# Performance work log

Hardware: AMD Instinct MI355X
Metric: run time of the kernel (lower is better)

The kernel has to match this reference:

```python
import jax, jax.numpy as jnp
import numpy as np


def setup_inputs() -> dict:
    key = jax.random.key(0)
    ks = jax.random.split(key, 16)
    s = 0.02
    return {
        "video": jax.random.normal(ks[0], (256, 10, 7, 7, 512), jnp.float32),
        "audio": jax.random.normal(ks[1], (10, 256, 128), jnp.float32),
        "Wv1": jax.random.normal(ks[2], (512, 512), jnp.float32) * s,
        "bv1": jnp.zeros((512,), jnp.float32),
        "Wa1": jax.random.normal(ks[3], (512, 128), jnp.float32) * s,
        "ba1": jnp.zeros((512,), jnp.float32),
        "Wb": jax.random.normal(ks[4], (256, 512), jnp.float32) * s,
        "bb": jnp.zeros((256,), jnp.float32),
        "Wc": jax.random.normal(ks[5], (512, 256), jnp.float32) * s,
        "bc": jnp.zeros((512,), jnp.float32),
        "Wv2": jax.random.normal(ks[6], (256, 512), jnp.float32) * s,
        "bv2": jnp.zeros((256,), jnp.float32),
        "Wa2": jax.random.normal(ks[7], (256, 128), jnp.float32) * s,
        "ba2": jnp.zeros((256,), jnp.float32),
        "Ws": jax.random.normal(ks[8], (1, 256), jnp.float32) * s,
        "bs": jnp.zeros((1,), jnp.float32),
    }


def reference(video, audio, Wv1, bv1, Wa1, ba1, Wb, bb, Wc, bc, Wv2, bv2, Wa2, ba2, Ws, bs):
    # video: [B, T, H, W, 512]; audio: [T, B, 128] (transposed inside, as in torch code)
    relu = jax.nn.relu
    audio = jnp.transpose(audio, (1, 0, 2))                  # [B, T, 128]
    B, T, H, W, Vd = video.shape
    BT, HW = B * T, H * W
    af = audio.reshape(BT, -1)                               # [BT, 128]
    vf = video.reshape(B, T, HW, Vd)                         # raw visual feature

    # channel attention
    aq1 = relu(af @ Wa1.T + ba1)[:, None, :]                 # [BT, 1, 512]
    vq1 = relu(vf @ Wv1.T + bv1).reshape(BT, HW, -1)         # [BT, 49, 512]
    avq = jnp.mean(aq1 * vq1, axis=-2)                       # [BT, 512]
    avq = relu(avq @ Wb.T + bb)                              # [BT, 256]
    c_att_maps = jax.nn.sigmoid(avq @ Wc.T + bc).reshape(B, T, 1, Vd)
    c_att = (vf * (c_att_maps + 1.0)).reshape(BT, HW, Vd)    # [BT, 49, 512]

    # spatial attention
    cq = relu(c_att @ Wv2.T + bv2)                           # [BT, 49, 256]
    aq2 = relu(af @ Wa2.T + ba2)[:, None, :]                 # [BT, 1, 256]
    logits = jnp.tanh((cq * aq2) @ Ws.T + bs)                # [BT, 49, 1]
    s_att = jax.nn.softmax(jnp.transpose(logits, (0, 2, 1)), axis=-1)  # [BT, 1, 49]

    out = jnp.matmul(s_att, c_att)                           # [BT, 1, 512]
    return out.reshape(B, T, Vd)
```

## Files before the change

kernel.cpp:

```cpp
#include <hip/hip_runtime.h>

typedef __bf16 bf16x8 __attribute__((ext_vector_type(8)));
typedef float f32x4 __attribute__((ext_vector_type(4)));

__device__ __forceinline__ unsigned short f2bf(float f) {
    union { float f; unsigned int u; } x; x.f = f;
    unsigned int r = x.u + 0x7FFFu + ((x.u >> 16) & 1u);
    return (unsigned short)(r >> 16);
}
__device__ __forceinline__ float bf2f(unsigned short v) {
    union { unsigned int u; float f; } x; x.u = ((unsigned int)v) << 16; return x.f;
}
__device__ __forceinline__ float bf2f_lo(unsigned int w) {
    union { unsigned int u; float f; } x; x.u = w << 16; return x.f;
}
__device__ __forceinline__ float bf2f_hi(unsigned int w) {
    union { unsigned int u; float f; } x; x.u = w & 0xffff0000u; return x.f;
}
__device__ __forceinline__ unsigned int cvt_pk_bf16(float lo, float hi) {
    unsigned int r;
    asm("v_cvt_pk_bf16_f32 %0, %1, %2" : "=v"(r) : "v"(lo), "v"(hi));
    return r;
}
__device__ __forceinline__ void async16(const void* g, void* l) {
    __builtin_amdgcn_global_load_lds(
        (const __attribute__((address_space(1))) unsigned int*)g,
        (__attribute__((address_space(3))) unsigned int*)l, 16, 0, 0);
}

__global__ __launch_bounds__(256) void k_prep(
    const float* __restrict__ Wv1, const float* __restrict__ Wv2,
    unsigned short* __restrict__ Wv1bf, unsigned short* __restrict__ Wv2bf)
{
    int idx = blockIdx.x * 256 + threadIdx.x;
    if (idx < 262144) {
        Wv1bf[idx] = f2bf(Wv1[idx]);
    } else {
        int j = idx - 262144;
        Wv2bf[j] = f2bf(Wv2[j]);
    }
}

__global__ __launch_bounds__(256) void k_prepv(
    const float* __restrict__ v, unsigned short* __restrict__ vbf)
{
    const size_t stride = (size_t)gridDim.x * 256;
    for (size_t c = (size_t)blockIdx.x * 256 + threadIdx.x; c < 8028160u; c += stride) {
        const float* p = v + c * 8;
        float4 a = *(const float4*)p;
        float4 b = *(const float4*)(p + 4);
        uint4 o;
        o.x = cvt_pk_bf16(a.x, a.y); o.y = cvt_pk_bf16(a.z, a.w);
        o.z = cvt_pk_bf16(b.x, b.y); o.w = cvt_pk_bf16(b.z, b.w);
        *(uint4*)(vbf + c * 8) = o;
    }
}

__global__ __launch_bounds__(256) void k_audio(
    const float* __restrict__ audio,
    const float* __restrict__ Wa1, const float* __restrict__ ba1,
    const float* __restrict__ Wa2, const float* __restrict__ ba2,
    float* __restrict__ aq1, float* __restrict__ aq2)
{
    __shared__ float afs[4][128];
    const int btBase = blockIdx.x * 4;
    const int tid = threadIdx.x;
    for (int i = tid; i < 512; i += 256) {
        int g = i >> 7, k = i & 127;
        int bt = btBase + g;
        int b = bt / 10, t = bt - b * 10;
        afs[g][k] = audio[(t * 256 + b) * 128 + k];
    }
    __syncthreads();
    const int c = tid;
    float a1a[4] = {0.f,0.f,0.f,0.f}, a1b[4] = {0.f,0.f,0.f,0.f}, a2[4] = {0.f,0.f,0.f,0.f};
    const float* w1a = Wa1 + c * 128;
    const float* w1b = Wa1 + (c + 256) * 128;
    const float* w2p = Wa2 + c * 128;
    for (int kk = 0; kk < 32; ++kk) {
        float4 va = *(const float4*)(w1a + kk * 4);
        float4 vb = *(const float4*)(w1b + kk * 4);
        float4 vc = *(const float4*)(w2p + kk * 4);
        float fa[4] = {va.x, va.y, va.z, va.w};
        float fb[4] = {vb.x, vb.y, vb.z, vb.w};
        float fc[4] = {vc.x, vc.y, vc.z, vc.w};
#pragma unroll
        for (int j = 0; j < 4; ++j) {
            int k = kk * 4 + j;
#pragma unroll
            for (int g = 0; g < 4; ++g) {
                float a = afs[g][k];
                a1a[g] += a * fa[j];
                a1b[g] += a * fb[j];
                a2[g]  += a * fc[j];
            }
        }
    }
    float b1a = ba1[c], b1b = ba1[c + 256], b2 = ba2[c];
#pragma unroll
    for (int g = 0; g < 4; ++g) {
        int bt = btBase + g;
        aq1[bt * 512 + c]       = fmaxf(a1a[g] + b1a, 0.f);
        aq1[bt * 512 + c + 256] = fmaxf(a1b[g] + b1b, 0.f);
        aq2[bt * 256 + c]       = fmaxf(a2[g] + b2, 0.f);
    }
}

__global__ __launch_bounds__(512) void k_chanatt_g(
    const unsigned short* __restrict__ videobf,
    const unsigned short* __restrict__ Wv1bf, const float* __restrict__ bv1,
    const float* __restrict__ aq1, float* __restrict__ avq)
{
    __shared__ unsigned short lds[2 * 12288];
    const int tid = threadIdx.x;
    const int wave = tid >> 6, lane = tid & 63, quad = lane >> 4, l16 = lane & 15;
    const int wm = wave >> 2, wn = wave & 3;
    const int mb = blockIdx.x >> 1, nb = blockIdx.x & 1;
    const int bt0 = mb * 2;

    auto stage = [&](int buf, int kt) {
        const int base = buf * 12288;
        {
            int row = tid >> 2, c = tid & 3;
            int hw = row & 63, btl = row >> 6;
            if (hw < 49) {
                async16(videobf + (size_t)(bt0 + btl) * 25088 + hw * 512
                                + kt * 32 + ((c ^ (row & 3)) << 3),
                        &lds[base + tid * 8]);
            }
        }
#pragma unroll
        for (int rep = 0; rep < 2; ++rep) {
            int q = tid + rep * 512;
            int row = q >> 2, c = q & 3;
            async16(Wv1bf + (size_t)((nb << 8) + row) * 512
                          + kt * 32 + ((c ^ (row & 3)) << 3),
                    &lds[base + 4096 + q * 8]);
        }
    };

    f32x4 acc[4][4];
#pragma unroll
    for (int mt = 0; mt < 4; ++mt)
#pragma unroll
        for (int nt = 0; nt < 4; ++nt)
            acc[mt][nt] = (f32x4){0.f, 0.f, 0.f, 0.f};

    stage(0, 0);
    __syncthreads();

    for (int kt = 0; kt < 16; ++kt) {
        int cur = kt & 1;
        if (kt < 15) stage(cur ^ 1, kt + 1);
        const int cb = cur * 12288;
        bf16x8 af[4];
#pragma unroll
        for (int mt = 0; mt < 4; ++mt) {
            int row = wm * 64 + mt * 16 + l16;
            af[mt] = *(const bf16x8*)&lds[cb + row * 32 + ((quad ^ (row & 3)) << 3)];
        }
#pragma unroll
        for (int nt = 0; nt < 4; ++nt) {
            int rowb = wn * 64 + nt * 16 + l16;
            bf16x8 bfr = *(const bf16x8*)&lds[cb + 4096 + rowb * 32 + ((quad ^ (rowb & 3)) << 3)];
#pragma unroll
            for (int mt = 0; mt < 4; ++mt)
                acc[mt][nt] = __builtin_amdgcn_mfma_f32_16x16x32_bf16(
                    af[mt], bfr, acc[mt][nt], 0, 0, 0);
        }
        __syncthreads();
    }

    const int bt = bt0 + wm;
#pragma unroll
    for (int nt = 0; nt < 4; ++nt) {
        int n = nb * 256 + wn * 64 + nt * 16 + l16;
        float bias = bv1[n];
        float s = 0.f;
#pragma unroll
        for (int mt = 0; mt < 4; ++mt)
#pragma unroll
            for (int r = 0; r < 4; ++r)
                if (mt < 3 || (quad == 0 && r == 0))
                    s += fmaxf(acc[mt][nt][r] + bias, 0.f);
        s += __shfl_xor(s, 16, 64);
        s += __shfl_xor(s, 32, 64);
        if (quad == 0) {
            avq[bt * 512 + n] = aq1[bt * 512 + n] * (s * (1.f / 49.f));
        }
    }
}

__global__ __launch_bounds__(256) void k_mlp(
    const float* __restrict__ avq,
    const float* __restrict__ Wb, const float* __restrict__ bb,
    const float* __restrict__ Wc, const float* __restrict__ bc,
    float* __restrict__ cmul)
{
    __shared__ float av[4][512];
    __shared__ float hid[4][256];
    const int btBase = blockIdx.x * 4;
    const int tid = threadIdx.x;
    for (int i = tid; i < 2048; i += 256) {
        int g = i >> 9, c = i & 511;
        av[g][c] = avq[(btBase + g) * 512 + c];
    }
    __syncthreads();
    {
        float a[4] = {0.f,0.f,0.f,0.f};
        const float* wrow = Wb + tid * 512;
        for (int kk = 0; kk < 128; ++kk) {
            float4 v = *(const float4*)(wrow + kk * 4);
            float w[4] = {v.x, v.y, v.z, v.w};
#pragma unroll
            for (int j = 0; j < 4; ++j)
#pragma unroll
                for (int g = 0; g < 4; ++g)
                    a[g] += av[g][kk * 4 + j] * w[j];
        }
        float bias = bb[tid];
#pragma unroll
        for (int g = 0; g < 4; ++g) hid[g][tid] = fmaxf(a[g] + bias, 0.f);
    }
    __syncthreads();
#pragma unroll
    for (int rep = 0; rep < 2; ++rep) {
        int c = tid + rep * 256;
        float a[4] = {0.f,0.f,0.f,0.f};
        const float* wrow = Wc + c * 256;
        for (int kk = 0; kk < 64; ++kk) {
            float4 v = *(const float4*)(wrow + kk * 4);
            float w[4] = {v.x, v.y, v.z, v.w};
#pragma unroll
            for (int j = 0; j < 4; ++j)
#pragma unroll
                for (int g = 0; g < 4; ++g)
                    a[g] += hid[g][kk * 4 + j] * w[j];
        }
        float bias = bc[c];
#pragma unroll
        for (int g = 0; g < 4; ++g) {
            float s = 1.f / (1.f + __expf(-(a[g] + bias)));
            cmul[(btBase + g) * 512 + c] = 1.f + s;
        }
    }
}

__global__ __launch_bounds__(512) void k_sgemm(
    const unsigned short* __restrict__ videobf,
    const float* __restrict__ cmul, const float* __restrict__ aq2,
    const unsigned short* __restrict__ Wv2bf, const float* __restrict__ bv2,
    const float* __restrict__ Wsp, const float* __restrict__ bsp,
    float* __restrict__ smw)
{
    __shared__ unsigned short lds[2 * 12288];
    __shared__ float zsh[8][64];
    const int tid = threadIdx.x;
    const int wave = tid >> 6, lane = tid & 63, quad = lane >> 4, l16 = lane & 15;
    const int wm = wave >> 2, wn = wave & 3;
    const int bt0 = blockIdx.x * 2;

    auto stage = [&](int buf, int kt) {
        const int base = buf * 12288;
        {
            int row = tid >> 2, c = tid & 3;
            int hw = row & 63, btl = row >> 6;
            int bt = bt0 + btl;
            if (hw < 49) {
                int k0 = kt * 32 + ((c ^ (row & 3)) << 3);
                uint4 v = *(const uint4*)(videobf + (size_t)bt * 25088 + hw * 512 + k0);
                const float* cp = cmul + bt * 512 + k0;
                float4 c0 = *(const float4*)cp;
                float4 c1 = *(const float4*)(cp + 4);
                uint4 o;
                o.x = cvt_pk_bf16(bf2f_lo(v.x) * c0.x, bf2f_hi(v.x) * c0.y);
                o.y = cvt_pk_bf16(bf2f_lo(v.y) * c0.z, bf2f_hi(v.y) * c0.w);
                o.z = cvt_pk_bf16(bf2f_lo(v.z) * c1.x, bf2f_hi(v.z) * c1.y);
                o.w = cvt_pk_bf16(bf2f_lo(v.w) * c1.z, bf2f_hi(v.w) * c1.w);
                *(uint4*)&lds[base + tid * 8] = o;
            }
        }
#pragma unroll
        for (int rep = 0; rep < 2; ++rep) {
            int q = tid + rep * 512;
            int row = q >> 2, c = q & 3;
            async16(Wv2bf + (size_t)row * 512 + kt * 32 + ((c ^ (row & 3)) << 3),
                    &lds[base + 4096 + q * 8]);
        }
    };

    f32x4 acc[4][4];
#pragma unroll
    for (int mt = 0; mt < 4; ++mt)
#pragma unroll
        for (int nt = 0; nt < 4; ++nt)
            acc[mt][nt] = (f32x4){0.f, 0.f, 0.f, 0.f};

    stage(0, 0);
    __syncthreads();

    for (int kt = 0; kt < 16; ++kt) {
        int cur = kt & 1;
        if (kt < 15) stage(cur ^ 1, kt + 1);
        const int cb = cur * 12288;
        bf16x8 af[4];
#pragma unroll
        for (int mt = 0; mt < 4; ++mt) {
            int row = wm * 64 + mt * 16 + l16;
            af[mt] = *(const bf16x8*)&lds[cb + row * 32 + ((quad ^ (row & 3)) << 3)];
        }
#pragma unroll
        for (int nt = 0; nt < 4; ++nt) {
            int rowb = wn * 64 + nt * 16 + l16;
            bf16x8 bfr = *(const bf16x8*)&lds[cb + 4096 + rowb * 32 + ((quad ^ (rowb & 3)) << 3)];
#pragma unroll
            for (int mt = 0; mt < 4; ++mt)
                acc[mt][nt] = __builtin_amdgcn_mfma_f32_16x16x32_bf16(
                    af[mt], bfr, acc[mt][nt], 0, 0, 0);
        }
        __syncthreads();
    }

    const int bt = bt0 + wm;
    float zp[16];
#pragma unroll
    for (int i = 0; i < 16; ++i) zp[i] = 0.f;
#pragma unroll
    for (int nt = 0; nt < 4; ++nt) {
        int n = wn * 64 + nt * 16 + l16;
        float bias = bv2[n];
        float co = aq2[bt * 256 + n] * Wsp[n];
#pragma unroll
        for (int mt = 0; mt < 4; ++mt)
#pragma unroll
            for (int r = 0; r < 4; ++r)
                zp[mt * 4 + r] += fmaxf(acc[mt][nt][r] + bias, 0.f) * co;
    }
#pragma unroll
    for (int i = 0; i < 16; ++i) {
        float v = zp[i];
        v += __shfl_xor(v, 1, 64);
        v += __shfl_xor(v, 2, 64);
        v += __shfl_xor(v, 4, 64);
        v += __shfl_xor(v, 8, 64);
        zp[i] = v;
    }
    if (l16 == 0) {
#pragma unroll
        for (int mt = 0; mt < 4; ++mt)
#pragma unroll
            for (int r = 0; r < 4; ++r)
                zsh[wave][mt * 16 + quad * 4 + r] = zp[mt * 4 + r];
    }
    __syncthreads();

    if (wn == 0) {
        int hw = lane;
        float z = zsh[wm * 4 + 0][hw] + zsh[wm * 4 + 1][hw]
                + zsh[wm * 4 + 2][hw] + zsh[wm * 4 + 3][hw] + bsp[0];
        float t = tanhf(z);
        float v = (hw < 49) ? t : -1e30f;
#pragma unroll
        for (int off = 32; off; off >>= 1) v = fmaxf(v, __shfl_xor(v, off, 64));
        float e = (hw < 49) ? __expf(t - v) : 0.f;
        float se = e;
#pragma unroll
        for (int off = 32; off; off >>= 1) se += __shfl_xor(se, off, 64);
        smw[bt * 64 + hw] = (hw < 49) ? (e / se) : 0.f;
    }
}

__global__ __launch_bounds__(256) void k_out(
    const unsigned short* __restrict__ videobf,
    const float* __restrict__ cmul, const float* __restrict__ smw,
    float* __restrict__ out)
{
    __shared__ float sm[49];
    const int bt = blockIdx.x;
    const int tid = threadIdx.x;
    if (tid < 49) sm[tid] = smw[bt * 64 + tid];
    __syncthreads();
    const unsigned short* vsrc = videobf + (size_t)bt * 25088;
#pragma unroll
    for (int rep = 0; rep < 2; ++rep) {
        int c = tid + rep * 256;
        float m = cmul[bt * 512 + c];
        float s = 0.f;
        for (int hw = 0; hw < 49; ++hw)
            s += sm[hw] * bf2f(vsrc[hw * 512 + c]);
        out[bt * 512 + c] = s * m;
    }
}

__global__ __launch_bounds__(256) void k_chanatt_fb(
    const float* __restrict__ video,
    const unsigned short* __restrict__ Wv1bf, const float* __restrict__ bv1,
    const float* __restrict__ aq1, float* __restrict__ avq)
{
    __shared__ unsigned short At[49 * 512];
    const int bt = blockIdx.x;
    const int tid = threadIdx.x;
    const int wave = tid >> 6, lane = tid & 63, quad = lane >> 4, l16 = lane & 15;
    const float* vsrc = video + (size_t)bt * 25088;

    for (int c = tid; c < 3136; c += 256) {
        int row = c >> 6, ch = c & 63;
        float4 a = *(const float4*)(vsrc + row * 512 + ch * 8);
        float4 b = *(const float4*)(vsrc + row * 512 + ch * 8 + 4);
        float f[8] = {a.x, a.y, a.z, a.w, b.x, b.y, b.z, b.w};
        unsigned int o[8];
#pragma unroll
        for (int j = 0; j < 8; ++j) o[j] = f2bf(f[j]);
        uint4 pack;
        pack.x = o[0] | (o[1] << 16); pack.y = o[2] | (o[3] << 16);
        pack.z = o[4] | (o[5] << 16); pack.w = o[6] | (o[7] << 16);
        int chs = ch ^ (row & 7);
        *(uint4*)(&At[row * 512 + chs * 8]) = pack;
    }
    __syncthreads();

    f32x4 acc[4][8];
#pragma unroll
    for (int mt = 0; mt < 4; ++mt)
#pragma unroll
        for (int nt = 0; nt < 8; ++nt)
            acc[mt][nt] = (f32x4){0.f, 0.f, 0.f, 0.f};

    for (int kk = 0; kk < 16; ++kk) {
        int chunk = kk * 4 + quad;
        bf16x8 afrag[4];
#pragma unroll
        for (int mt = 0; mt < 4; ++mt) {
            int m = ((mt == 3) ? 33 : mt * 16) + l16;
            int chs = chunk ^ (m & 7);
            afrag[mt] = *(const bf16x8*)(&At[m * 512 + chs * 8]);
        }
        int koff = chunk * 8;
#pragma unroll
        for (int nt = 0; nt < 8; ++nt) {
            int n = (wave * 8 + nt) * 16 + l16;
            bf16x8 bfrag = *(const bf16x8*)(Wv1bf + n * 512 + koff);
#pragma unroll
            for (int mt = 0; mt < 4; ++mt)
                acc[mt][nt] = __builtin_amdgcn_mfma_f32_16x16x32_bf16(
                    afrag[mt], bfrag, acc[mt][nt], 0, 0, 0);
        }
    }

#pragma unroll
    for (int nt = 0; nt < 8; ++nt) {
        int n = (wave * 8 + nt) * 16 + l16;
        float bias = bv1[n];
        float s = 0.f;
#pragma unroll
        for (int mt = 0; mt < 4; ++mt)
#pragma unroll
            for (int r = 0; r < 4; ++r)
                if (mt < 3 || (quad == 3 && r == 3))
                    s += fmaxf(acc[mt][nt][r] + bias, 0.f);
        s += __shfl_xor(s, 16, 64);
        s += __shfl_xor(s, 32, 64);
        if (quad == 0) {
            float vm = s * (1.f / 49.f);
            avq[bt * 512 + n] = aq1[bt * 512 + n] * vm;
        }
    }
}

__global__ __launch_bounds__(256) void k_spatial_fb(
    const float* __restrict__ video,
    const float* __restrict__ cmul, const float* __restrict__ aq2,
    const unsigned short* __restrict__ Wv2bf, const float* __restrict__ bv2,
    const float* __restrict__ Wsp, const float* __restrict__ bsp,
    float* __restrict__ out)
{
    __shared__ unsigned short Ct[49 * 512];
    __shared__ float w2[256];
    __shared__ float zbuf[4][64];
    __shared__ float smwl[64];
    const int bt = blockIdx.x;
    const int tid = threadIdx.x;
    const int wave = tid >> 6, lane = tid & 63, quad = lane >> 4, l16 = lane & 15;
    const float* vsrc = video + (size_t)bt * 25088;
    const float* cm = cmul + bt * 512;

    for (int c = tid; c < 3136; c += 256) {
        int row = c >> 6, ch = c & 63;
        float4 a = *(const float4*)(vsrc + row * 512 + ch * 8);
        float4 b = *(const float4*)(vsrc + row * 512 + ch * 8 + 4);
        float f[8] = {a.x, a.y, a.z, a.w, b.x, b.y, b.z, b.w};
        float4 m0 = *(const float4*)(cm + ch * 8);
        float4 m1 = *(const float4*)(cm + ch * 8 + 4);
        float mm[8] = {m0.x, m0.y, m0.z, m0.w, m1.x, m1.y, m1.z, m1.w};
        unsigned int o[8];
#pragma unroll
        for (int j = 0; j < 8; ++j) o[j] = f2bf(f[j] * mm[j]);
        uint4 pack;
        pack.x = o[0] | (o[1] << 16); pack.y = o[2] | (o[3] << 16);
        pack.z = o[4] | (o[5] << 16); pack.w = o[6] | (o[7] << 16);
        int chs = ch ^ (row & 7);
        *(uint4*)(&Ct[row * 512 + chs * 8]) = pack;
    }
    w2[tid] = aq2[bt * 256 + tid] * Wsp[tid];
    if (lane >= 49) zbuf[wave][lane] = 0.f;
    __syncthreads();

    f32x4 acc[4][4];
#pragma unroll
    for (int mt = 0; mt < 4; ++mt)
#pragma unroll
        for (int nt = 0; nt < 4; ++nt)
            acc[mt][nt] = (f32x4){0.f, 0.f, 0.f, 0.f};

    for (int kk = 0; kk < 16; ++kk) {
        int chunk = kk * 4 + quad;
        bf16x8 afrag[4];
#pragma unroll
        for (int mt = 0; mt < 4; ++mt) {
            int m = ((mt == 3) ? 33 : mt * 16) + l16;
            int chs = chunk ^ (m & 7);
            afrag[mt] = *(const bf16x8*)(&Ct[m * 512 + chs * 8]);
        }
        int koff = chunk * 8;
#pragma unroll
        for (int nt = 0; nt < 4; ++nt) {
            int n = (wave * 4 + nt) * 16 + l16;
            bf16x8 bfrag = *(const bf16x8*)(Wv2bf + n * 512 + koff);
#pragma unroll
            for (int mt = 0; mt < 4; ++mt)
                acc[mt][nt] = __builtin_amdgcn_mfma_f32_16x16x32_bf16(
                    afrag[mt], bfrag, acc[mt][nt], 0, 0, 0);
        }
    }

    float zp[16];
#pragma unroll
    for (int i = 0; i < 16; ++i) zp[i] = 0.f;
#pragma unroll
    for (int nt = 0; nt < 4; ++nt) {
        int n = (wave * 4 + nt) * 16 + l16;
        float bias = bv2[n];
        float wnc = w2[n];
#pragma unroll
        for (int mt = 0; mt < 4; ++mt)
#pragma unroll
            for (int r = 0; r < 4; ++r)
                zp[mt * 4 + r] += fmaxf(acc[mt][nt][r] + bias, 0.f) * wnc;
    }
#pragma unroll
    for (int i = 0; i < 16; ++i) {
        float v = zp[i];
        v += __shfl_xor(v, 1, 64);
        v += __shfl_xor(v, 2, 64);
        v += __shfl_xor(v, 4, 64);
        v += __shfl_xor(v, 8, 64);
        zp[i] = v;
    }
    if (l16 == 0) {
#pragma unroll
        for (int mt = 0; mt < 4; ++mt)
#pragma unroll
            for (int r = 0; r < 4; ++r)
                if (mt < 3 || (quad == 3 && r == 3)) {
                    int row = ((mt == 3) ? 33 : mt * 16) + quad * 4 + r;
                    zbuf[wave][row] = zp[mt * 4 + r];
                }
    }
    __syncthreads();

    if (wave == 0) {
        int hw = lane;
        float z = zbuf[0][hw] + zbuf[1][hw] + zbuf[2][hw] + zbuf[3][hw] + bsp[0];
        float t = tanhf(z);
        float v = (hw < 49) ? t : -1e30f;
#pragma unroll
        for (int off = 32; off; off >>= 1) v = fmaxf(v, __shfl_xor(v, off, 64));
        float e = (hw < 49) ? __expf(t - v) : 0.f;
        float se = e;
#pragma unroll
        for (int off = 32; off; off >>= 1) se += __shfl_xor(se, off, 64);
        smwl[hw] = e / se;
    }
    __syncthreads();

#pragma unroll
    for (int rep = 0; rep < 2; ++rep) {
        int cidx = tid + rep * 256;
        int chb = cidx >> 3, jj = cidx & 7;
        float s = 0.f;
        for (int hw = 0; hw < 49; ++hw) {
            int chs = chb ^ (hw & 7);
            s += smwl[hw] * bf2f(Ct[hw * 512 + chs * 8 + jj]);
        }
        out[bt * 512 + cidx] = s;
    }
}

extern "C" void kernel_launch(void* const* d_in, const int* in_sizes, int n_in,
                              void* d_out, int out_size, void* d_ws, size_t ws_size,
                              hipStream_t stream) {
    const float* video = (const float*)d_in[0];
    const float* audio = (const float*)d_in[1];
    const float* Wv1 = (const float*)d_in[2];
    const float* bv1 = (const float*)d_in[3];
    const float* Wa1 = (const float*)d_in[4];
    const float* ba1 = (const float*)d_in[5];
    const float* Wb  = (const float*)d_in[6];
    const float* bb  = (const float*)d_in[7];
    const float* Wc  = (const float*)d_in[8];
    const float* bc  = (const float*)d_in[9];
    const float* Wv2 = (const float*)d_in[10];
    const float* bv2 = (const float*)d_in[11];
    const float* Wa2 = (const float*)d_in[12];
    const float* ba2 = (const float*)d_in[13];
    const float* Wsp = (const float*)d_in[14];
    const float* bsp = (const float*)d_in[15];
    float* out = (float*)d_out;

    const size_t NEED = 147587072u;
    if (ws_size >= NEED) {
        unsigned short* videobf = (unsigned short*)d_ws;
        unsigned short* Wv1bf = videobf + 64225280;
        unsigned short* Wv2bf = Wv1bf + 262144;
        float* fbase = (float*)(Wv2bf + 131072);
        float* aq1  = fbase;
        float* aq2  = aq1 + 1310720;
        float* avq  = aq2 + 655360;
        float* cmul = avq + 1310720;
        float* smw  = aq1;

        k_prep<<<1536, 256, 0, stream>>>(Wv1, Wv2, Wv1bf, Wv2bf);
        k_prepv<<<4096, 256, 0, stream>>>(video, videobf);
        k_audio<<<640, 256, 0, stream>>>(audio, Wa1, ba1, Wa2, ba2, aq1, aq2);
        k_chanatt_g<<<2560, 512, 0, stream>>>(videobf, Wv1bf, bv1, aq1, avq);
        k_mlp<<<640, 256, 0, stream>>>(avq, Wb, bb, Wc, bc, cmul);
        k_sgemm<<<1280, 512, 0, stream>>>(videobf, cmul, aq2, Wv2bf, bv2, Wsp, bsp, smw);
        k_out<<<2560, 256, 0, stream>>>(videobf, cmul, smw, out);
    } else {
        float* ws = (float*)d_ws;
        float* aq1  = ws;
        float* aq2  = aq1 + 1310720;
        float* avq  = aq2 + 655360;
        float* cmul = avq + 1310720;
        unsigned short* Wv1bf = (unsigned short*)(cmul + 1310720);
        unsigned short* Wv2bf = Wv1bf + 262144;

        k_prep<<<1536, 256, 0, stream>>>(Wv1, Wv2, Wv1bf, Wv2bf);
        k_audio<<<640, 256, 0, stream>>>(audio, Wa1, ba1, Wa2, ba2, aq1, aq2);
        k_chanatt_fb<<<2560, 256, 0, stream>>>(video, Wv1bf, bv1, aq1, avq);
        k_mlp<<<640, 256, 0, stream>>>(avq, Wb, bb, Wc, bc, cmul);
        k_spatial_fb<<<2560, 256, 0, stream>>>(video, cmul, aq2, Wv2bf, bv2, Wsp, bsp, out);
    }
}
```

Before: 757.0 us.

## Fuse prep kernels and move output weighting into spatial GEMM kernel

Merges the weight conversion, video bf16 conversion and audio projection kernels into one launch with a block-range dispatch. Folds the final softmax-weighted sum over spatial positions into the spatial GEMM kernel, so k_out and the smw round trip are gone. It also splits the A-tile staging in the spatial GEMM into register load and LDS write phases around the MFMA loop to overlap global loads with compute. This removes launches and one full re-read pass with its own kernel, at the cost of a longer tail in the GEMM blocks.

```diff
diff --git a/kernel.cpp b/kernel.cpp
--- a/kernel.cpp
+++ b/kernel.cpp
@@ -26,6 +26,391 @@
     __builtin_amdgcn_global_load_lds(
         (const __attribute__((address_space(1))) unsigned int*)g,
         (__attribute__((address_space(3))) unsigned int*)l, 16, 0, 0);
+}
+
+__global__ __launch_bounds__(256) void k_front(
+    const float* __restrict__ video, unsigned short* __restrict__ vbf,
+    const float* __restrict__ Wv1, const float* __restrict__ Wv2,
+    unsigned short* __restrict__ Wv1bf, unsigned short* __restrict__ Wv2bf,
+    const float* __restrict__ audio,
+    const float* __restrict__ Wa1, const float* __restrict__ ba1,
+    const float* __restrict__ Wa2, const float* __restrict__ ba2,
+    float* __restrict__ aq1, float* __restrict__ aq2)
+{
+    const int b = blockIdx.x;
+    const int tid = threadIdx.x;
+    if (b < 4096) {
+        const size_t stride = (size_t)4096 * 256;
+        for (size_t c = (size_t)b * 256 + tid; c < 8028160u; c += stride) {
+            const float* p = video + c * 8;
+            float4 a = *(const float4*)p;
+            float4 bb4 = *(const float4*)(p + 4);
+            uint4 o;
+            o.x = cvt_pk_bf16(a.x, a.y); o.y = cvt_pk_bf16(a.z, a.w);
+            o.z = cvt_pk_bf16(bb4.x, bb4.y); o.w = cvt_pk_bf16(bb4.z, bb4.w);
+            *(uint4*)(vbf + c * 8) = o;
+        }
+        return;
+    }
+    if (b < 4480) {
+        int base = (b - 4096) * 1024 + tid;
+#pragma unroll
+        for (int r = 0; r < 4; ++r) {
+            int idx = base + r * 256;
+            if (idx < 262144) Wv1bf[idx] = f2bf(Wv1[idx]);
+            else              Wv2bf[idx - 262144] = f2bf(Wv2[idx - 262144]);
+        }
+        return;
+    }
+    __shared__ float afs[4][128];
+    const int btBase = (b - 4480) * 4;
+    for (int i = tid; i < 512; i += 256) {
+        int g = i >> 7, k = i & 127;
+        int bt = btBase + g;
+        int bb_ = bt / 10, t = bt - bb_ * 10;
+        afs[g][k] = audio[(t * 256 + bb_) * 128 + k];
+    }
+    __syncthreads();
+    const int c = tid;
+    float a1a[4] = {0.f,0.f,0.f,0.f}, a1b[4] = {0.f,0.f,0.f,0.f}, a2[4] = {0.f,0.f,0.f,0.f};
+    const float* w1a = Wa1 + c * 128;
+    const float* w1b = Wa1 + (c + 256) * 128;
+    const float* w2p = Wa2 + c * 128;
+    for (int kk = 0; kk < 32; ++kk) {
+        float4 va = *(const float4*)(w1a + kk * 4);
+        float4 vb = *(const float4*)(w1b + kk * 4);
+        float4 vc = *(const float4*)(w2p + kk * 4);
+        float fa[4] = {va.x, va.y, va.z, va.w};
+        float fb[4] = {vb.x, vb.y, vb.z, vb.w};
+        float fc[4] = {vc.x, vc.y, vc.z, vc.w};
+#pragma unroll
+        for (int j = 0; j < 4; ++j) {
+            int k = kk * 4 + j;
+#pragma unroll
+            for (int g = 0; g < 4; ++g) {
+                float a = afs[g][k];
+                a1a[g] += a * fa[j];
+                a1b[g] += a * fb[j];
+                a2[g]  += a * fc[j];
+            }
+        }
+    }
+    float b1a = ba1[c], b1b = ba1[c + 256], b2 = ba2[c];
+#pragma unroll
+    for (int g = 0; g < 4; ++g) {
+        int bt = btBase + g;
+        aq1[bt * 512 + c]       = fmaxf(a1a[g] + b1a, 0.f);
+        aq1[bt * 512 + c + 256] = fmaxf(a1b[g] + b1b, 0.f);
+        aq2[bt * 256 + c]       = fmaxf(a2[g] + b2, 0.f);
+    }
+}
+
+__global__ __launch_bounds__(512) void k_chanatt_g(
+    const unsigned short* __restrict__ videobf,
+    const unsigned short* __restrict__ Wv1bf, const float* __restrict__ bv1,
+    const float* __restrict__ aq1, float* __restrict__ avq)
+{
+    __shared__ unsigned short lds[2 * 12288];
+    const int tid = threadIdx.x;
+    const int wave = tid >> 6, lane = tid & 63, quad = lane >> 4, l16 = lane & 15;
+    const int wm = wave >> 2, wn = wave & 3;
+    const int mb = blockIdx.x >> 1, nb = blockIdx.x & 1;
+    const int bt0 = mb * 2;
+
+    auto stage = [&](int buf, int kt) {
+        const int base = buf * 12288;
+        {
+            int row = tid >> 2, c = tid & 3;
+            int hw = row & 63, btl = row >> 6;
+            if (hw < 49) {
+                async16(videobf + (size_t)(bt0 + btl) * 25088 + hw * 512
+                                + kt * 32 + ((c ^ (row & 3)) << 3),
+                        &lds[base + tid * 8]);
+            }
+        }
+#pragma unroll
+        for (int rep = 0; rep < 2; ++rep) {
+            int q = tid + rep * 512;
+            int row = q >> 2, c = q & 3;
+            async16(Wv1bf + (size_t)((nb << 8) + row) * 512
+                          + kt * 32 + ((c ^ (row & 3)) << 3),
+                    &lds[base + 4096 + q * 8]);
+        }
+    };
+
+    f32x4 acc[4][4];
+#pragma unroll
+    for (int mt = 0; mt < 4; ++mt)
+#pragma unroll
+        for (int nt = 0; nt < 4; ++nt)
+            acc[mt][nt] = (f32x4){0.f, 0.f, 0.f, 0.f};
+
+    stage(0, 0);
+    __syncthreads();
+
+    for (int kt = 0; kt < 16; ++kt) {
+        int cur = kt & 1;
+        if (kt < 15) stage(cur ^ 1, kt + 1);
+        const int cb = cur * 12288;
+        bf16x8 af[4];
+#pragma unroll
+        for (int mt = 0; mt < 4; ++mt) {
+            int row = wm * 64 + mt * 16 + l16;
+            af[mt] = *(const bf16x8*)&lds[cb + row * 32 + ((quad ^ (row & 3)) << 3)];
+        }
+#pragma unroll
+        for (int nt = 0; nt < 4; ++nt) {
+            int rowb = wn * 64 + nt * 16 + l16;
+            bf16x8 bfr = *(const bf16x8*)&lds[cb + 4096 + rowb * 32 + ((quad ^ (rowb & 3)) << 3)];
+#pragma unroll
+            for (int mt = 0; mt < 4; ++mt)
+                acc[mt][nt] = __builtin_amdgcn_mfma_f32_16x16x32_bf16(
+                    af[mt], bfr, acc[mt][nt], 0, 0, 0);
+        }
+        __syncthreads();
+    }
+
+    const int bt = bt0 + wm;
+#pragma unroll
+    for (int nt = 0; nt < 4; ++nt) {
+        int n = nb * 256 + wn * 64 + nt * 16 + l16;
+        float bias = bv1[n];
+        float s = 0.f;
+#pragma unroll
+        for (int mt = 0; mt < 4; ++mt)
+#pragma unroll
+            for (int r = 0; r < 4; ++r)
+                if (mt < 3 || (quad == 0 && r == 0))
+                    s += fmaxf(acc[mt][nt][r] + bias, 0.f);
+        s += __shfl_xor(s, 16, 64);
+        s += __shfl_xor(s, 32, 64);
+        if (quad == 0) {
+            avq[bt * 512 + n] = aq1[bt * 512 + n] * (s * (1.f / 49.f));
+        }
+    }
+}
+
+__global__ __launch_bounds__(256) void k_mlp(
+    const float* __restrict__ avq,
+    const float* __restrict__ Wb, const float* __restrict__ bb,
+    const float* __restrict__ Wc, const float* __restrict__ bc,
+    float* __restrict__ cmul)
+{
+    __shared__ float av[4][512];
+    __shared__ float hid[4][256];
+    const int btBase = blockIdx.x * 4;
+    const int tid = threadIdx.x;
+    for (int i = tid; i < 2048; i += 256) {
+        int g = i >> 9, c = i & 511;
+        av[g][c] = avq[(btBase + g) * 512 + c];
+    }
+    __syncthreads();
+    {
+        float a[4] = {0.f,0.f,0.f,0.f};
+        const float* wrow = Wb + tid * 512;
+        for (int kk = 0; kk < 128; ++kk) {
+            float4 v = *(const float4*)(wrow + kk * 4);
+            float w[4] = {v.x, v.y, v.z, v.w};
+#pragma unroll
+            for (int j = 0; j < 4; ++j)
+#pragma unroll
+                for (int g = 0; g < 4; ++g)
+                    a[g] += av[g][kk * 4 + j] * w[j];
+        }
+        float bias = bb[tid];
+#pragma unroll
+        for (int g = 0; g < 4; ++g) hid[g][tid] = fmaxf(a[g] + bias, 0.f);
+    }
+    __syncthreads();
+#pragma unroll
+    for (int rep = 0; rep < 2; ++rep) {
+        int c = tid + rep * 256;
+        float a[4] = {0.f,0.f,0.f,0.f};
+        const float* wrow = Wc + c * 256;
+        for (int kk = 0; kk < 64; ++kk) {
+            float4 v = *(const float4*)(wrow + kk * 4);
+            float w[4] = {v.x, v.y, v.z, v.w};
+#pragma unroll
+            for (int j = 0; j < 4; ++j)
+#pragma unroll
+                for (int g = 0; g < 4; ++g)
+                    a[g] += hid[g][kk * 4 + j] * w[j];
+        }
+        float bias = bc[c];
+#pragma unroll
+        for (int g = 0; g < 4; ++g) {
+            float s = 1.f / (1.f + __expf(-(a[g] + bias)));
+            cmul[(btBase + g) * 512 + c] = 1.f + s;
+        }
+    }
+}
+
+__global__ __launch_bounds__(512) void k_sgemm(
+    const unsigned short* __restrict__ videobf,
+    const float* __restrict__ cmul, const float* __restrict__ aq2,
+    const unsigned short* __restrict__ Wv2bf, const float* __restrict__ bv2,
+    const float* __restrict__ Wsp, const float* __restrict__ bsp,
+    float* __restrict__ out)
+{
+    __shared__ unsigned short lds[2 * 12288];
+    __shared__ float zsh[8][64];
+    __shared__ float smloc[2][64];
+    const int tid = threadIdx.x;
+    const int wave = tid >> 6, lane = tid & 63, quad = lane >> 4, l16 = lane & 15;
+    const int wm = wave >> 2, wn = wave & 3;
+    const int bt0 = blockIdx.x * 2;
+
+    const int arow = tid >> 2, ac = tid & 3;
+    const int ahw = arow & 63, abtl = arow >> 6;
+    const bool aok = (ahw < 49);
+    const int aswz = (ac ^ (arow & 3)) << 3;
+    const unsigned short* avsrc = videobf + (size_t)(bt0 + abtl) * 25088 + ahw * 512;
+    const float* acm = cmul + (bt0 + abtl) * 512;
+    uint4 vreg;
+    float4 c0reg, c1reg;
+
+    auto aload = [&](int kt) {
+        if (aok) {
+            int k0 = kt * 32 + aswz;
+            vreg  = *(const uint4*)(avsrc + k0);
+            c0reg = *(const float4*)(acm + k0);
+            c1reg = *(const float4*)(acm + k0 + 4);
+        }
+    };
+    auto awrite = [&](int buf) {
+        if (aok) {
+            uint4 o;
+            o.x = cvt_pk_bf16(bf2f_lo(vreg.x) * c0reg.x, bf2f_hi(vreg.x) * c0reg.y);
+            o.y = cvt_pk_bf16(bf2f_lo(vreg.y) * c0reg.z, bf2f_hi(vreg.y) * c0reg.w);
+            o.z = cvt_pk_bf16(bf2f_lo(vreg.z) * c1reg.x, bf2f_hi(vreg.z) * c1reg.y);
+            o.w = cvt_pk_bf16(bf2f_lo(vreg.w) * c1reg.z, bf2f_hi(vreg.w) * c1reg.w);
+            *(uint4*)&lds[buf * 12288 + tid * 8] = o;
+        }
+    };
+    auto stageB = [&](int buf, int kt) {
+#pragma unroll
+        for (int rep = 0; rep < 2; ++rep) {
+            int q = tid + rep * 512;
+            int row = q >> 2, c = q & 3;
+            async16(Wv2bf + (size_t)row * 512 + kt * 32 + ((c ^ (row & 3)) << 3),
+                    &lds[buf * 12288 + 4096 + q * 8]);
+        }
+    };
+
+    f32x4 acc[4][4];
+#pragma unroll
+    for (int mt = 0; mt < 4; ++mt)
+#pragma unroll
+        for (int nt = 0; nt < 4; ++nt)
+            acc[mt][nt] = (f32x4){0.f, 0.f, 0.f, 0.f};
+
+    aload(0);
+    stageB(0, 0);
+    awrite(0);
+    __syncthreads();
+
+    for (int kt = 0; kt < 16; ++kt) {
+        int cur = kt & 1;
+        if (kt < 15) { aload(kt + 1); stageB(cur ^ 1, kt + 1); }
+        const int cb = cur * 12288;
+        bf16x8 af[4];
+#pragma unroll
+        for (int mt = 0; mt < 4; ++mt) {
+            int row = wm * 64 + mt * 16 + l16;
+            af[mt] = *(const bf16x8*)&lds[cb + row * 32 + ((quad ^ (row & 3)) << 3)];
+        }
+#pragma unroll
+        for (int nt = 0; nt < 4; ++nt) {
+            int rowb = wn * 64 + nt * 16 + l16;
+            bf16x8 bfr = *(const bf16x8*)&lds[cb + 4096 + rowb * 32 + ((quad ^ (rowb & 3)) << 3)];
+#pragma unroll
+            for (int mt = 0; mt < 4; ++mt)
+                acc[mt][nt] = __builtin_amdgcn_mfma_f32_16x16x32_bf16(
+                    af[mt], bfr, acc[mt][nt], 0, 0, 0);
+        }
+        if (kt < 15) awrite(cur ^ 1);
+        __syncthreads();
+    }
+
+    const int bt = bt0 + wm;
+    float zp[16];
+#pragma unroll
+    for (int i = 0; i < 16; ++i) zp[i] = 0.f;
+#pragma unroll
+    for (int nt = 0; nt < 4; ++nt) {
+        int n = wn * 64 + nt * 16 + l16;
+        float bias = bv2[n];
+        float co = aq2[bt * 256 + n] * Wsp[n];
+#pragma unroll
+        for (int mt = 0; mt < 4; ++mt)
+#pragma unroll
+            for (int r = 0; r < 4; ++r)
+                zp[mt * 4 + r] += fmaxf(acc[mt][nt][r] + bias, 0.f) * co;
+    }
+#pragma unroll
+    for (int i = 0; i < 16; ++i) {
+        float v = zp[i];
+        v += __shfl_xor(v, 1, 64);
+        v += __shfl_xor(v, 2, 64);
+        v += __shfl_xor(v, 4, 64);
+        v += __shfl_xor(v, 8, 64);
+        zp[i] = v;
+    }
+    if (l16 == 0) {
+#pragma unroll
+        for (int mt = 0; mt < 4; ++mt)
+#pragma unroll
+            for (int r = 0; r < 4; ++r)
+                zsh[wave][mt * 16 + quad * 4 + r] = zp[mt * 4 + r];
+    }
+    __syncthreads();
+
+    if (wn == 0) {
+        int hw = lane;
+        float z = zsh[wm * 4 + 0][hw] + zsh[wm * 4 + 1][hw]
+                + zsh[wm * 4 + 2][hw] + zsh[wm * 4 + 3][hw] + bsp[0];
+        float t = tanhf(z);
+        float v = (hw < 49) ? t : -1e30f;
+#pragma unroll
+        for (int off = 32; off; off >>= 1) v = fmaxf(v, __shfl_xor(v, off, 64));
+        float e = (hw < 49) ? __expf(t - v) : 0.f;
+        float se = e;
+#pragma unroll
+        for (int off = 32; off; off >>= 1) se += __shfl_xor(se, off, 64);
+        smloc[wm][hw] = (hw < 49) ? (e / se) : 0.f;
+    }
+    __syncthreads();
+
+    {
+        int g = tid >> 2, part = tid & 3;
+        int btl = g >> 6, cg = g & 63;
+        const unsigned short* vs = videobf + (size_t)(bt0 + btl) * 25088 + cg * 8;
+        float s[8];
+#pragma unroll
+        for (int j = 0; j < 8; ++j) s[j] = 0.f;
+        for (int hw = part; hw < 49; hw += 4) {
+            float w = smloc[btl][hw];
+            uint4 v = *(const uint4*)(vs + hw * 512);
+            s[0] += w * bf2f_lo(v.x); s[1] += w * bf2f_hi(v.x);
+            s[2] += w * bf2f_lo(v.y); s[3] += w * bf2f_hi(v.y);
+            s[4] += w * bf2f_lo(v.z); s[5] += w * bf2f_hi(v.z);
+            s[6] += w * bf2f_lo(v.w); s[7] += w * bf2f_hi(v.w);
+        }
+#pragma unroll
+        for (int j = 0; j < 8; ++j) {
+            s[j] += __shfl_xor(s[j], 1, 64);
+            s[j] += __shfl_xor(s[j], 2, 64);
+        }
+        if (part == 0) {
+            const float* cm = cmul + (bt0 + btl) * 512 + cg * 8;
+            float4 m0 = *(const float4*)cm;
+            float4 m1 = *(const float4*)(cm + 4);
+            float mm[8] = {m0.x, m0.y, m0.z, m0.w, m1.x, m1.y, m1.z, m1.w};
+            float* op = out + (bt0 + btl) * 512 + cg * 8;
+#pragma unroll
+            for (int j = 0; j < 8; ++j) op[j] = s[j] * mm[j];
+        }
+    }
 }
 
 __global__ __launch_bounds__(256) void k_prep(
@@ -38,21 +423,6 @@
     } else {
         int j = idx - 262144;
         Wv2bf[j] = f2bf(Wv2[j]);
-    }
-}
-
-__global__ __launch_bounds__(256) void k_prepv(
-    const float* __restrict__ v, unsigned short* __restrict__ vbf)
-{
-    const size_t stride = (size_t)gridDim.x * 256;
-    for (size_t c = (size_t)blockIdx.x * 256 + threadIdx.x; c < 8028160u; c += stride) {
-        const float* p = v + c * 8;
-        float4 a = *(const float4*)p;
-        float4 b = *(const float4*)(p + 4);
-        uint4 o;
-        o.x = cvt_pk_bf16(a.x, a.y); o.y = cvt_pk_bf16(a.z, a.w);
-        o.z = cvt_pk_bf16(b.x, b.y); o.w = cvt_pk_bf16(b.z, b.w);
-        *(uint4*)(vbf + c * 8) = o;
     }
 }
 
@@ -103,292 +473,6 @@
         aq1[bt * 512 + c]       = fmaxf(a1a[g] + b1a, 0.f);
         aq1[bt * 512 + c + 256] = fmaxf(a1b[g] + b1b, 0.f);
         aq2[bt * 256 + c]       = fmaxf(a2[g] + b2, 0.f);
-    }
-}
-
-__global__ __launch_bounds__(512) void k_chanatt_g(
-    const unsigned short* __restrict__ videobf,
-    const unsigned short* __restrict__ Wv1bf, const float* __restrict__ bv1,
-    const float* __restrict__ aq1, float* __restrict__ avq)
-{
-    __shared__ unsigned short lds[2 * 12288];
-    const int tid = threadIdx.x;
-    const int wave = tid >> 6, lane = tid & 63, quad = lane >> 4, l16 = lane & 15;
-    const int wm = wave >> 2, wn = wave & 3;
-    const int mb = blockIdx.x >> 1, nb = blockIdx.x & 1;
-    const int bt0 = mb * 2;
-
-    auto stage = [&](int buf, int kt) {
-        const int base = buf * 12288;
-        {
-            int row = tid >> 2, c = tid & 3;
-            int hw = row & 63, btl = row >> 6;
-            if (hw < 49) {
-                async16(videobf + (size_t)(bt0 + btl) * 25088 + hw * 512
-                                + kt * 32 + ((c ^ (row & 3)) << 3),
-                        &lds[base + tid * 8]);
-            }
-        }
-#pragma unroll
-        for (int rep = 0; rep < 2; ++rep) {
-            int q = tid + rep * 512;
-            int row = q >> 2, c = q & 3;
-            async16(Wv1bf + (size_t)((nb << 8) + row) * 512
-                          + kt * 32 + ((c ^ (row & 3)) << 3),
-                    &lds[base + 4096 + q * 8]);
-        }
-    };
-
-    f32x4 acc[4][4];
-#pragma unroll
-    for (int mt = 0; mt < 4; ++mt)
-#pragma unroll
-        for (int nt = 0; nt < 4; ++nt)
-            acc[mt][nt] = (f32x4){0.f, 0.f, 0.f, 0.f};
-
-    stage(0, 0);
-    __syncthreads();
-
-    for (int kt = 0; kt < 16; ++kt) {
-        int cur = kt & 1;
-        if (kt < 15) stage(cur ^ 1, kt + 1);
-        const int cb = cur * 12288;
-        bf16x8 af[4];
-#pragma unroll
-        for (int mt = 0; mt < 4; ++mt) {
-            int row = wm * 64 + mt * 16 + l16;
-            af[mt] = *(const bf16x8*)&lds[cb + row * 32 + ((quad ^ (row & 3)) << 3)];
-        }
-#pragma unroll
-        for (int nt = 0; nt < 4; ++nt) {
-            int rowb = wn * 64 + nt * 16 + l16;
-            bf16x8 bfr = *(const bf16x8*)&lds[cb + 4096 + rowb * 32 + ((quad ^ (rowb & 3)) << 3)];
-#pragma unroll
-            for (int mt = 0; mt < 4; ++mt)
-                acc[mt][nt] = __builtin_amdgcn_mfma_f32_16x16x32_bf16(
-                    af[mt], bfr, acc[mt][nt], 0, 0, 0);
-        }
-        __syncthreads();
-    }
-
-    const int bt = bt0 + wm;
-#pragma unroll
-    for (int nt = 0; nt < 4; ++nt) {
-        int n = nb * 256 + wn * 64 + nt * 16 + l16;
-        float bias = bv1[n];
-        float s = 0.f;
-#pragma unroll
-        for (int mt = 0; mt < 4; ++mt)
-#pragma unroll
-            for (int r = 0; r < 4; ++r)
-                if (mt < 3 || (quad == 0 && r == 0))
-                    s += fmaxf(acc[mt][nt][r] + bias, 0.f);
-        s += __shfl_xor(s, 16, 64);
-        s += __shfl_xor(s, 32, 64);
-        if (quad == 0) {
-            avq[bt * 512 + n] = aq1[bt * 512 + n] * (s * (1.f / 49.f));
-        }
-    }
-}
-
-__global__ __launch_bounds__(256) void k_mlp(
-    const float* __restrict__ avq,
-    const float* __restrict__ Wb, const float* __restrict__ bb,
-    const float* __restrict__ Wc, const float* __restrict__ bc,
-    float* __restrict__ cmul)
-{
-    __shared__ float av[4][512];
-    __shared__ float hid[4][256];
-    const int btBase = blockIdx.x * 4;
-    const int tid = threadIdx.x;
-    for (int i = tid; i < 2048; i += 256) {
-        int g = i >> 9, c = i & 511;
-        av[g][c] = avq[(btBase + g) * 512 + c];
-    }
-    __syncthreads();
-    {
-        float a[4] = {0.f,0.f,0.f,0.f};
-        const float* wrow = Wb + tid * 512;
-        for (int kk = 0; kk < 128; ++kk) {
-            float4 v = *(const float4*)(wrow + kk * 4);
-            float w[4] = {v.x, v.y, v.z, v.w};
-#pragma unroll
-            for (int j = 0; j < 4; ++j)
-#pragma unroll
-                for (int g = 0; g < 4; ++g)
-                    a[g] += av[g][kk * 4 + j] * w[j];
-        }
-        float bias = bb[tid];
-#pragma unroll
-        for (int g = 0; g < 4; ++g) hid[g][tid] = fmaxf(a[g] + bias, 0.f);
-    }
-    __syncthreads();
-#pragma unroll
-    for (int rep = 0; rep < 2; ++rep) {
-        int c = tid + rep * 256;
-        float a[4] = {0.f,0.f,0.f,0.f};
-        const float* wrow = Wc + c * 256;
-        for (int kk = 0; kk < 64; ++kk) {
-            float4 v = *(const float4*)(wrow + kk * 4);
-            float w[4] = {v.x, v.y, v.z, v.w};
-#pragma unroll
-            for (int j = 0; j < 4; ++j)
-#pragma unroll
-                for (int g = 0; g < 4; ++g)
-                    a[g] += hid[g][kk * 4 + j] * w[j];
-        }
-        float bias = bc[c];
-#pragma unroll
-        for (int g = 0; g < 4; ++g) {
-            float s = 1.f / (1.f + __expf(-(a[g] + bias)));
-            cmul[(btBase + g) * 512 + c] = 1.f + s;
-        }
-    }
-}
-
-__global__ __launch_bounds__(512) void k_sgemm(
-    const unsigned short* __restrict__ videobf,
-    const float* __restrict__ cmul, const float* __restrict__ aq2,
-    const unsigned short* __restrict__ Wv2bf, const float* __restrict__ bv2,
-    const float* __restrict__ Wsp, const float* __restrict__ bsp,
-    float* __restrict__ smw)
-{
-    __shared__ unsigned short lds[2 * 12288];
-    __shared__ float zsh[8][64];
-    const int tid = threadIdx.x;
-    const int wave = tid >> 6, lane = tid & 63, quad = lane >> 4, l16 = lane & 15;
-    const int wm = wave >> 2, wn = wave & 3;
-    const int bt0 = blockIdx.x * 2;
-
-    auto stage = [&](int buf, int kt) {
-        const int base = buf * 12288;
-        {
-            int row = tid >> 2, c = tid & 3;
-            int hw = row & 63, btl = row >> 6;
-            int bt = bt0 + btl;
-            if (hw < 49) {
-                int k0 = kt * 32 + ((c ^ (row & 3)) << 3);
-                uint4 v = *(const uint4*)(videobf + (size_t)bt * 25088 + hw * 512 + k0);
-                const float* cp = cmul + bt * 512 + k0;
-                float4 c0 = *(const float4*)cp;
-                float4 c1 = *(const float4*)(cp + 4);
-                uint4 o;
-                o.x = cvt_pk_bf16(bf2f_lo(v.x) * c0.x, bf2f_hi(v.x) * c0.y);
-                o.y = cvt_pk_bf16(bf2f_lo(v.y) * c0.z, bf2f_hi(v.y) * c0.w);
-                o.z = cvt_pk_bf16(bf2f_lo(v.z) * c1.x, bf2f_hi(v.z) * c1.y);
-                o.w = cvt_pk_bf16(bf2f_lo(v.w) * c1.z, bf2f_hi(v.w) * c1.w);
-                *(uint4*)&lds[base + tid * 8] = o;
-            }
-        }
-#pragma unroll
-        for (int rep = 0; rep < 2; ++rep) {
-            int q = tid + rep * 512;
-            int row = q >> 2, c = q & 3;
-            async16(Wv2bf + (size_t)row * 512 + kt * 32 + ((c ^ (row & 3)) << 3),
-                    &lds[base + 4096 + q * 8]);
-        }
-    };
-
-    f32x4 acc[4][4];
-#pragma unroll
-    for (int mt = 0; mt < 4; ++mt)
-#pragma unroll
-        for (int nt = 0; nt < 4; ++nt)
-            acc[mt][nt] = (f32x4){0.f, 0.f, 0.f, 0.f};
-
-    stage(0, 0);
-    __syncthreads();
-
-    for (int kt = 0; kt < 16; ++kt) {
-        int cur = kt & 1;
-        if (kt < 15) stage(cur ^ 1, kt + 1);
-        const int cb = cur * 12288;
-        bf16x8 af[4];
-#pragma unroll
-        for (int mt = 0; mt < 4; ++mt) {
-            int row = wm * 64 + mt * 16 + l16;
-            af[mt] = *(const bf16x8*)&lds[cb + row * 32 + ((quad ^ (row & 3)) << 3)];
-        }
-#pragma unroll
-        for (int nt = 0; nt < 4; ++nt) {
-            int rowb = wn * 64 + nt * 16 + l16;
-            bf16x8 bfr = *(const bf16x8*)&lds[cb + 4096 + rowb * 32 + ((quad ^ (rowb & 3)) << 3)];
-#pragma unroll
-            for (int mt = 0; mt < 4; ++mt)
-                acc[mt][nt] = __builtin_amdgcn_mfma_f32_16x16x32_bf16(
-                    af[mt], bfr, acc[mt][nt], 0, 0, 0);
-        }
-        __syncthreads();
-    }
-
-    const int bt = bt0 + wm;
-    float zp[16];
-#pragma unroll
-    for (int i = 0; i < 16; ++i) zp[i] = 0.f;
-#pragma unroll
-    for (int nt = 0; nt < 4; ++nt) {
-        int n = wn * 64 + nt * 16 + l16;
-        float bias = bv2[n];
-        float co = aq2[bt * 256 + n] * Wsp[n];
-#pragma unroll
-        for (int mt = 0; mt < 4; ++mt)
-#pragma unroll
-            for (int r = 0; r < 4; ++r)
-                zp[mt * 4 + r] += fmaxf(acc[mt][nt][r] + bias, 0.f) * co;
-    }
-#pragma unroll
-    for (int i = 0; i < 16; ++i) {
-        float v = zp[i];
-        v += __shfl_xor(v, 1, 64);
-        v += __shfl_xor(v, 2, 64);
-        v += __shfl_xor(v, 4, 64);
-        v += __shfl_xor(v, 8, 64);
-        zp[i] = v;
-    }
-    if (l16 == 0) {
-#pragma unroll
-        for (int mt = 0; mt < 4; ++mt)
-#pragma unroll
-            for (int r = 0; r < 4; ++r)
-                zsh[wave][mt * 16 + quad * 4 + r] = zp[mt * 4 + r];
-    }
-    __syncthreads();
-
-    if (wn == 0) {
-        int hw = lane;
-        float z = zsh[wm * 4 + 0][hw] + zsh[wm * 4 + 1][hw]
-                + zsh[wm * 4 + 2][hw] + zsh[wm * 4 + 3][hw] + bsp[0];
-        float t = tanhf(z);
-        float v = (hw < 49) ? t : -1e30f;
-#pragma unroll
-        for (int off = 32; off; off >>= 1) v = fmaxf(v, __shfl_xor(v, off, 64));
-        float e = (hw < 49) ? __expf(t - v) : 0.f;
-        float se = e;
-#pragma unroll
-        for (int off = 32; off; off >>= 1) se += __shfl_xor(se, off, 64);
-        smw[bt * 64 + hw] = (hw < 49) ? (e / se) : 0.f;
-    }
-}
-
-__global__ __launch_bounds__(256) void k_out(
-    const unsigned short* __restrict__ videobf,
-    const float* __restrict__ cmul, const float* __restrict__ smw,
-    float* __restrict__ out)
-{
-    __shared__ float sm[49];
-    const int bt = blockIdx.x;
-    const int tid = threadIdx.x;
-    if (tid < 49) sm[tid] = smw[bt * 64 + tid];
-    __syncthreads();
-    const unsigned short* vsrc = videobf + (size_t)bt * 25088;
-#pragma unroll
-    for (int rep = 0; rep < 2; ++rep) {
-        int c = tid + rep * 256;
-        float m = cmul[bt * 512 + c];
-        float s = 0.f;
-        for (int hw = 0; hw < 49; ++hw)
-            s += sm[hw] * bf2f(vsrc[hw * 512 + c]);
-        out[bt * 512 + c] = s * m;
     }
 }
 
@@ -627,15 +711,12 @@
         float* aq2  = aq1 + 1310720;
         float* avq  = aq2 + 655360;
         float* cmul = avq + 1310720;
-        float* smw  = aq1;
-
-        k_prep<<<1536, 256, 0, stream>>>(Wv1, Wv2, Wv1bf, Wv2bf);
-        k_prepv<<<4096, 256, 0, stream>>>(video, videobf);
-        k_audio<<<640, 256, 0, stream>>>(audio, Wa1, ba1, Wa2, ba2, aq1, aq2);
+
+        k_front<<<5120, 256, 0, stream>>>(video, videobf, Wv1, Wv2, Wv1bf, Wv2bf,
+                                          audio, Wa1, ba1, Wa2, ba2, aq1, aq2);
         k_chanatt_g<<<2560, 512, 0, stream>>>(videobf, Wv1bf, bv1, aq1, avq);
         k_mlp<<<640, 256, 0, stream>>>(avq, Wb, bb, Wc, bc, cmul);
-        k_sgemm<<<1280, 512, 0, stream>>>(videobf, cmul, aq2, Wv2bf, bv2, Wsp, bsp, smw);
-        k_out<<<2560, 256, 0, stream>>>(videobf, cmul, smw, out);
+        k_sgemm<<<1280, 512, 0, stream>>>(videobf, cmul, aq2, Wv2bf, bv2, Wsp, bsp, out);
     } else {
         float* ws = (float*)d_ws;
         float* aq1  = ws;
```

Result: faster. 739.5 us (-2.3%).
